# Performance work log

Measured on AMD Instinct MI355X. Metric: run time of the kernel, lower is better.

The kernel has to match this reference:

```python
import jax, jax.numpy as jnp
import numpy as np

B, C_IN, C_OUT, H, W = 2, 64, 32, 80, 80


def conv1x1(x, w, b):
    # x: [B, Cin, H, W], w: [Cout, Cin], b: [Cout]
    return jnp.einsum('bchw,oc->bohw', x, w) + b[None, :, None, None]


def setup_inputs() -> dict:
    key = jax.random.key(0)
    ks = jax.random.split(key, 5)
    scale = 0.02  # keep dot products moderate since exp() is unscaled (no max-subtract)
    return {
        'input_x': jax.random.normal(ks[0], (B, C_IN, H, W), dtype=jnp.float32),
        'w_g': jax.random.normal(ks[1], (C_OUT, C_IN), dtype=jnp.float32) * scale,
        'b_g': jnp.zeros((C_OUT,), dtype=jnp.float32),
        'w_phi': jax.random.normal(ks[2], (C_OUT, C_IN), dtype=jnp.float32) * scale,
        'b_phi': jnp.zeros((C_OUT,), dtype=jnp.float32),
        'w_theta': jax.random.normal(ks[3], (C_OUT, C_IN), dtype=jnp.float32) * scale,
        'b_theta': jnp.zeros((C_OUT,), dtype=jnp.float32),
        'w_y': jax.random.normal(ks[4], (C_IN, C_OUT), dtype=jnp.float32) * scale,
        'b_y': jnp.zeros((C_IN,), dtype=jnp.float32),
    }


def reference(input_x, w_g, b_g, w_phi, b_phi, w_theta, b_theta, w_y, b_y):
    batch = input_x.shape[0]
    g = conv1x1(input_x, w_g, b_g)          # [B, Cout, H, W]
    phi = conv1x1(input_x, w_phi, b_phi)    # [B, Cout, H, W]
    theta = conv1x1(input_x, w_theta, b_theta)
    # Faithful to torch: raw reshape (row-major reinterpretation), NOT a transpose
    g_x = g.reshape(batch, -1, C_OUT)        # [B, HW, Cout]
    theta_x = theta.reshape(batch, -1, C_OUT)
    phi_x = phi.reshape(batch, -1, C_OUT)
    f = jnp.einsum('bnc,bmc->bnm', theta_x, phi_x)  # [B, HW, HW]
    # nltype=0: unscaled exp / row-sum normalization (no max subtraction, faithful)
    f = jnp.exp(f)
    f_softmax = f / jnp.sum(f, axis=-1, keepdims=True)
    y = jnp.einsum('bnm,bmc->bnc', f_softmax, g_x)  # [B, HW, Cout]
    y = y.reshape(batch, C_OUT, H, W)
    z = conv1x1(y, w_y, b_y)                 # [B, Cin, H, W]
    return z
```

## Files before the change

kernel.cpp:

```cpp
#include <hip/hip_runtime.h>
#include <hip/hip_bf16.h>

#define BATCH 2
#define CIN   64
#define COUT  32
#define HW    6400
#define PB    (COUT*HW)
#define XB    (CIN*HW)
#define KSPLIT 10
#define LOG2E 1.4426950408889634f

typedef __attribute__((ext_vector_type(8))) short  bf16x8;
typedef __attribute__((ext_vector_type(4))) float  f32x4;

typedef unsigned short ushort;
typedef unsigned int   uint;

__device__ inline uint pk2(float a, float b) {
  __hip_bfloat162 h = __float22bfloat162_rn(make_float2(a, b));
  union { __hip_bfloat162 h2; uint u; } cv; cv.h2 = h;
  return cv.u;
}
__device__ inline uint pkt(float a, float b) {
  return (__float_as_uint(b) & 0xFFFF0000u) | (__float_as_uint(a) >> 16);
}

#define MFMA16(a, bop, c) __builtin_amdgcn_mfma_f32_16x16x32_bf16((a), (bop), (c), 0, 0, 0)

__global__ __launch_bounds__(128) void conv3_kernel(
    const float* __restrict__ x,
    const float* __restrict__ w0, const float* __restrict__ bb0,
    const float* __restrict__ w1, const float* __restrict__ bb1,
    const float* __restrict__ w2, const float* __restrict__ bb2,
    ushort* __restrict__ T_hi, ushort* __restrict__ P_hi,
    ushort* __restrict__ Gt_hi) {
  const int which = blockIdx.y >> 1;
  const int oh    = blockIdx.y & 1;
  const float* w  = (which == 0) ? w0 : (which == 1) ? w1 : w2;
  const float* bv = (which == 0) ? bb0 : (which == 1) ? bb1 : bb2;
  const int b = blockIdx.z;
  const int s = blockIdx.x * 128 + threadIdx.x;

  __shared__ float wsm[16 * CIN];
  for (int i = threadIdx.x; i < 16 * CIN; i += 128)
    wsm[i] = w[oh * 16 * CIN + i];
  __syncthreads();

  float xr[CIN];
#pragma unroll
  for (int c = 0; c < CIN; ++c) xr[c] = x[b * XB + c * HW + s];

  for (int oi = 0; oi < 16; ++oi) {
    const int o = oh * 16 + oi;
    const float4* wr = (const float4*)&wsm[oi * CIN];
    float acc = 0.f;
#pragma unroll
    for (int q = 0; q < CIN / 4; ++q) {
      float4 wv = wr[q];
      acc += wv.x * xr[4*q] + wv.y * xr[4*q+1] + wv.z * xr[4*q+2] + wv.w * xr[4*q+3];
    }
    acc += bv[o];
    if (which == 0) acc *= LOG2E;
    const ushort hb = (ushort)(pk2(acc, 0.f) & 0xFFFFu);
    if (which == 2) {
      const int m  = o * 200 + (s >> 5);
      const int np = (m & ~31) + 16*((m>>3)&1) + 8*((m>>2)&1)
                   + 4*((m>>4)&1) + (m & 3);
      Gt_hi[b * PB + (s & 31) * HW + np] = hb;
    } else {
      const int f = b * PB + o * HW + s;
      if (which == 0) T_hi[f] = hb; else P_hi[f] = hb;
    }
  }
}

__global__ __launch_bounds__(256, 3) void attn_kernel(
    const ushort* __restrict__ T_hi, const ushort* __restrict__ P_hi,
    const ushort* __restrict__ Gt_hi,
    float* __restrict__ Yp,
    float* __restrict__ Dp) {
  const int b     = blockIdx.z;
  const int ks    = blockIdx.y;
  const int q_blk = blockIdx.x;
  const int tid   = threadIdx.x;
  const int w     = tid >> 6;
  const int lane  = tid & 63;
  const int l15   = lane & 15;
  const int g     = lane >> 4;

  __shared__ float yl[4 * 32 * 33 + 4 * 32];

  const int niter = 640 / 128;
  const int kbase = ks * 640 + w * 32;

  bf16x8 t_hi[4];
#pragma unroll
  for (int s2 = 0; s2 < 4; ++s2) {
    const int qrow = q_blk * 64 + s2 * 16 + l15;
    t_hi[s2] = *(const bf16x8*)&T_hi[b * PB + qrow * 32 + g * 8];
  }

  union { uint u[4]; bf16x8 v; } g2u;
  {
    const uint ov = (l15 == 0) ? 0x3F803F80u : 0u;
    g2u.u[0] = ov; g2u.u[1] = ov; g2u.u[2] = ov; g2u.u[3] = ov;
  }
  const bf16x8 g2 = g2u.v;

  const ushort* pg = P_hi + b * PB + (kbase + l15) * 32 + g * 8;
  const ushort* gg = Gt_hi + b * PB + l15 * HW + kbase + g * 8;

  f32x4 acc0[4] = {{0,0,0,0},{0,0,0,0},{0,0,0,0},{0,0,0,0}};
  f32x4 acc1[4] = {{0,0,0,0},{0,0,0,0},{0,0,0,0},{0,0,0,0}};
  f32x4 acc2[4] = {{0,0,0,0},{0,0,0,0},{0,0,0,0},{0,0,0,0}};

  bf16x8 pa = *(const bf16x8*)pg;
  bf16x8 pb = *(const bf16x8*)(pg + 512);
  bf16x8 g0 = *(const bf16x8*)gg;
  bf16x8 g1 = *(const bf16x8*)(gg + 16 * HW);

  for (int i = 0; i < niter; ++i) {
    bf16x8 pan, pbn, g0n, g1n;
    if (i + 1 < niter) {
      const ushort* pgn = pg + (i + 1) * 4096;
      const ushort* ggn = gg + (i + 1) * 128;
      pan = *(const bf16x8*)pgn;
      pbn = *(const bf16x8*)(pgn + 512);
      g0n = *(const bf16x8*)ggn;
      g1n = *(const bf16x8*)(ggn + 16 * HW);
    }

#pragma unroll
    for (int s2 = 0; s2 < 4; ++s2) {
      f32x4 sa = {0.f,0.f,0.f,0.f};
      f32x4 sb = {0.f,0.f,0.f,0.f};
      sa = MFMA16(pa, t_hi[s2], sa);
      sb = MFMA16(pb, t_hi[s2], sb);

      const float ea0 = __builtin_amdgcn_exp2f(sa[0]);
      const float ea1 = __builtin_amdgcn_exp2f(sa[1]);
      const float ea2 = __builtin_amdgcn_exp2f(sa[2]);
      const float ea3 = __builtin_amdgcn_exp2f(sa[3]);
      const float eb0 = __builtin_amdgcn_exp2f(sb[0]);
      const float eb1 = __builtin_amdgcn_exp2f(sb[1]);
      const float eb2 = __builtin_amdgcn_exp2f(sb[2]);
      const float eb3 = __builtin_amdgcn_exp2f(sb[3]);

      union { uint u[4]; bf16x8 v; } ph;
      ph.u[0] = pkt(ea0, ea1); ph.u[1] = pkt(ea2, ea3);
      ph.u[2] = pkt(eb0, eb1); ph.u[3] = pkt(eb2, eb3);

      acc0[s2] = MFMA16(ph.v, g0, acc0[s2]);
      acc1[s2] = MFMA16(ph.v, g1, acc1[s2]);
      acc2[s2] = MFMA16(ph.v, g2, acc2[s2]);
    }

    if (i + 1 < niter) { pa = pan; pb = pbn; g0 = g0n; g1 = g1n; }
  }

  float* dl = yl + 4 * 32 * 33;
  const int c  = tid & 31;
  const int q0 = tid >> 5;

#pragma unroll
  for (int p = 0; p < 2; ++p) {
    __syncthreads();
#pragma unroll
    for (int sl = 0; sl < 2; ++sl) {
      const int s2 = p * 2 + sl;
#pragma unroll
      for (int r = 0; r < 4; ++r) {
        yl[(w * 32 + sl * 16 + 4 * g + r) * 33 + l15]      = acc0[s2][r];
        yl[(w * 32 + sl * 16 + 4 * g + r) * 33 + 16 + l15] = acc1[s2][r];
      }
      if (l15 == 0) {
#pragma unroll
        for (int r = 0; r < 4; ++r)
          dl[w * 32 + sl * 16 + 4 * g + r] = acc2[s2][r];
      }
    }
    __syncthreads();

#pragma unroll
    for (int rr = 0; rr < 4; ++rr) {
      const int row = rr * 8 + q0;
      float y = 0.f, d = 0.f;
#pragma unroll
      for (int k2 = 0; k2 < 4; ++k2) {
        y += yl[(k2 * 32 + row) * 33 + c];
        d += dl[k2 * 32 + row];
      }
      const int qrow = q_blk * 64 + p * 32 + row;
      Yp[((size_t)(ks * BATCH + b)) * PB + qrow * 32 + c] = y;
      if (c == 0) Dp[((size_t)(ks * BATCH + b)) * HW + qrow] = d;
    }
  }
}

__global__ __launch_bounds__(128) void conv_out_kernel(
    const float* __restrict__ Yp, const float* __restrict__ Dp,
    const float* __restrict__ wy, const float* __restrict__ by,
    float* __restrict__ z) {
  const int b  = blockIdx.z;
  const int ih = blockIdx.y;
  const int s  = blockIdx.x * 128 + threadIdx.x;

  __shared__ float wsm[32 * COUT];
  for (int i = threadIdx.x; i < 32 * COUT; i += 128)
    wsm[i] = wy[ih * 32 * COUT + i];
  __syncthreads();

  float yr[COUT];
#pragma unroll
  for (int o = 0; o < COUT; ++o) {
    const int f = o * HW + s;
    const int n = f >> 5;
    float y = 0.f, d = 0.f;
#pragma unroll
    for (int ksi = 0; ksi < KSPLIT; ++ksi) {
      y += Yp[((size_t)(ksi * BATCH + b)) * PB + f];
      d += Dp[((size_t)(ksi * BATCH + b)) * HW + n];
    }
    yr[o] = y / d;
  }

  for (int ii = 0; ii < 32; ++ii) {
    const int i = ih * 32 + ii;
    const float4* wr = (const float4*)&wsm[ii * COUT];
    float acc = 0.f;
#pragma unroll
    for (int q = 0; q < COUT / 4; ++q) {
      float4 wv = wr[q];
      acc += wv.x * yr[4*q] + wv.y * yr[4*q+1] + wv.z * yr[4*q+2] + wv.w * yr[4*q+3];
    }
    z[(size_t)b * XB + i * HW + s] = acc + by[i];
  }
}

extern "C" void kernel_launch(void* const* d_in, const int* in_sizes, int n_in,
                              void* d_out, int out_size, void* d_ws, size_t ws_size,
                              hipStream_t stream) {
  const float* x       = (const float*)d_in[0];
  const float* w_g     = (const float*)d_in[1];
  const float* b_g     = (const float*)d_in[2];
  const float* w_phi   = (const float*)d_in[3];
  const float* b_phi   = (const float*)d_in[4];
  const float* w_theta = (const float*)d_in[5];
  const float* b_theta = (const float*)d_in[6];
  const float* w_y     = (const float*)d_in[7];
  const float* b_y     = (const float*)d_in[8];
  float* z = (float*)d_out;

  char* base = (char*)d_ws;
  const size_t BF = (size_t)BATCH * PB * sizeof(ushort);
  ushort* T_hi  = (ushort*)(base);
  ushort* P_hi  = (ushort*)(base + 1 * BF);
  ushort* Gt_hi = (ushort*)(base + 2 * BF);
  float*  Yp    = (float*)(base + 3 * BF);
  float*  Dp    = (float*)(base + 3 * BF +
                           (size_t)KSPLIT * BATCH * PB * sizeof(float));

  conv3_kernel<<<dim3(50, 6, BATCH), 128, 0, stream>>>(
      x, w_theta, b_theta, w_phi, b_phi, w_g, b_g,
      T_hi, P_hi, Gt_hi);
  attn_kernel<<<dim3(100, KSPLIT, BATCH), 256, 0, stream>>>(
      T_hi, P_hi, Gt_hi, Yp, Dp);
  conv_out_kernel<<<dim3(50, 2, BATCH), 128, 0, stream>>>(Yp, Dp, w_y, b_y, z);
}
```

Baseline: 57.07 us.

## Remove split-K in attention, reduce over full key range inside 512-thread blocks

```diff
diff --git a/kernel.cpp b/kernel.cpp
--- a/kernel.cpp
+++ b/kernel.cpp
@@ -7,7 +7,6 @@
 #define HW    6400
 #define PB    (COUT*HW)
 #define XB    (CIN*HW)
-#define KSPLIT 10
 #define LOG2E 1.4426950408889634f
 
 typedef __attribute__((ext_vector_type(8))) short  bf16x8;
@@ -74,13 +73,11 @@
   }
 }
 
-__global__ __launch_bounds__(256, 3) void attn_kernel(
+__global__ __launch_bounds__(512, 2) void attn_kernel(
     const ushort* __restrict__ T_hi, const ushort* __restrict__ P_hi,
     const ushort* __restrict__ Gt_hi,
-    float* __restrict__ Yp,
-    float* __restrict__ Dp) {
-  const int b     = blockIdx.z;
-  const int ks    = blockIdx.y;
+    float* __restrict__ Y) {
+  const int b     = blockIdx.y;
   const int q_blk = blockIdx.x;
   const int tid   = threadIdx.x;
   const int w     = tid >> 6;
@@ -88,10 +85,10 @@
   const int l15   = lane & 15;
   const int g     = lane >> 4;
 
-  __shared__ float yl[4 * 32 * 33 + 4 * 32];
-
-  const int niter = 640 / 128;
-  const int kbase = ks * 640 + w * 32;
+  __shared__ float yl[8 * 16 * 33 + 8 * 16];
+
+  const int niter = 25;
+  const int kbase = w * 32;
 
   bf16x8 t_hi[4];
 #pragma unroll
@@ -122,8 +119,8 @@
   for (int i = 0; i < niter; ++i) {
     bf16x8 pan, pbn, g0n, g1n;
     if (i + 1 < niter) {
-      const ushort* pgn = pg + (i + 1) * 4096;
-      const ushort* ggn = gg + (i + 1) * 128;
+      const ushort* pgn = pg + (i + 1) * 8192;
+      const ushort* ggn = gg + (i + 1) * 256;
       pan = *(const bf16x8*)pgn;
       pbn = *(const bf16x8*)(pgn + 512);
       g0n = *(const bf16x8*)ggn;
@@ -158,49 +155,42 @@
     if (i + 1 < niter) { pa = pan; pb = pbn; g0 = g0n; g1 = g1n; }
   }
 
-  float* dl = yl + 4 * 32 * 33;
-  const int c  = tid & 31;
-  const int q0 = tid >> 5;
-
-#pragma unroll
-  for (int p = 0; p < 2; ++p) {
+  float* dl = yl + 8 * 16 * 33;
+  const int c   = tid & 31;
+  const int row = (tid >> 5) & 15;
+
+#pragma unroll
+  for (int p = 0; p < 4; ++p) {
     __syncthreads();
-#pragma unroll
-    for (int sl = 0; sl < 2; ++sl) {
-      const int s2 = p * 2 + sl;
+    {
+      const int s2 = p;
 #pragma unroll
       for (int r = 0; r < 4; ++r) {
-        yl[(w * 32 + sl * 16 + 4 * g + r) * 33 + l15]      = acc0[s2][r];
-        yl[(w * 32 + sl * 16 + 4 * g + r) * 33 + 16 + l15] = acc1[s2][r];
+        yl[(w * 16 + 4 * g + r) * 33 + l15]      = acc0[s2][r];
+        yl[(w * 16 + 4 * g + r) * 33 + 16 + l15] = acc1[s2][r];
       }
       if (l15 == 0) {
 #pragma unroll
         for (int r = 0; r < 4; ++r)
-          dl[w * 32 + sl * 16 + 4 * g + r] = acc2[s2][r];
+          dl[w * 16 + 4 * g + r] = acc2[s2][r];
       }
     }
     __syncthreads();
 
-#pragma unroll
-    for (int rr = 0; rr < 4; ++rr) {
-      const int row = rr * 8 + q0;
-      float y = 0.f, d = 0.f;
-#pragma unroll
-      for (int k2 = 0; k2 < 4; ++k2) {
-        y += yl[(k2 * 32 + row) * 33 + c];
-        d += dl[k2 * 32 + row];
-      }
-      const int qrow = q_blk * 64 + p * 32 + row;
-      Yp[((size_t)(ks * BATCH + b)) * PB + qrow * 32 + c] = y;
-      if (c == 0) Dp[((size_t)(ks * BATCH + b)) * HW + qrow] = d;
-    }
+    float y = 0.f, d = 0.f;
+#pragma unroll
+    for (int k2 = 0; k2 < 8; ++k2) {
+      y += yl[(k2 * 16 + row) * 33 + c];
+      d += dl[k2 * 16 + row];
+    }
+    const int qrow = q_blk * 64 + p * 16 + row;
+    Y[(size_t)b * PB + qrow * 32 + c] = y / d;
   }
 }
 
 __global__ __launch_bounds__(128) void conv_out_kernel(
-    const float* __restrict__ Yp, const float* __restrict__ Dp,
-    const float* __restrict__ wy, const float* __restrict__ by,
-    float* __restrict__ z) {
+    const float* __restrict__ Y, const float* __restrict__ wy,
+    const float* __restrict__ by, float* __restrict__ z) {
   const int b  = blockIdx.z;
   const int ih = blockIdx.y;
   const int s  = blockIdx.x * 128 + threadIdx.x;
@@ -212,17 +202,8 @@
 
   float yr[COUT];
 #pragma unroll
-  for (int o = 0; o < COUT; ++o) {
-    const int f = o * HW + s;
-    const int n = f >> 5;
-    float y = 0.f, d = 0.f;
-#pragma unroll
-    for (int ksi = 0; ksi < KSPLIT; ++ksi) {
-      y += Yp[((size_t)(ksi * BATCH + b)) * PB + f];
-      d += Dp[((size_t)(ksi * BATCH + b)) * HW + n];
-    }
-    yr[o] = y / d;
-  }
+  for (int o = 0; o < COUT; ++o)
+    yr[o] = Y[(size_t)b * PB + o * HW + s];
 
   for (int ii = 0; ii < 32; ++ii) {
     const int i = ih * 32 + ii;
@@ -256,14 +237,12 @@
   ushort* T_hi  = (ushort*)(base);
   ushort* P_hi  = (ushort*)(base + 1 * BF);
   ushort* Gt_hi = (ushort*)(base + 2 * BF);
-  float*  Yp    = (float*)(base + 3 * BF);
-  float*  Dp    = (float*)(base + 3 * BF +
-                           (size_t)KSPLIT * BATCH * PB * sizeof(float));
+  float*  Y     = (float*)(base + 3 * BF);
 
   conv3_kernel<<<dim3(50, 6, BATCH), 128, 0, stream>>>(
       x, w_theta, b_theta, w_phi, b_phi, w_g, b_g,
       T_hi, P_hi, Gt_hi);
-  attn_kernel<<<dim3(100, KSPLIT, BATCH), 256, 0, stream>>>(
-      T_hi, P_hi, Gt_hi, Yp, Dp);
-  conv_out_kernel<<<dim3(50, 2, BATCH), 128, 0, stream>>>(Yp, Dp, w_y, b_y, z);
-}
+  attn_kernel<<<dim3(100, BATCH), 512, 0, stream>>>(
+      T_hi, P_hi, Gt_hi, Y);
+  conv_out_kernel<<<dim3(50, 2, BATCH), 128, 0, stream>>>(Y, w_y, b_y, z);
+}
```

Result: faster. 49.38 us (-13.5%).
